# Optimization experiments

Hardware: AMD Instinct MI355X
Metric: run time of the kernel (lower is better)

## Reference

```python
import jax, jax.numpy as jnp
import numpy as np

IN_FEATURES = 2048
OUT_FEATURES = 4096
NUM_SHIFTS = 10  # perms


def setup_inputs() -> dict:
    key = jax.random.key(0)
    kx, kw = jax.random.split(key)
    x = jax.random.normal(kx, (4, 2048, IN_FEATURES), dtype=jnp.float32)
    # nn.Linear weight: (out_features, in_features), Kaiming-uniform-ish init
    bound = 1.0 / np.sqrt(IN_FEATURES)
    W = jax.random.uniform(kw, (OUT_FEATURES, IN_FEATURES), dtype=jnp.float32,
                           minval=-bound, maxval=bound)
    return {"x": x, "W": W}


def _combined_weight(W):
    # Wt: (in, out). Sum of all weight variants; sum_i(x @ W_i) == x @ sum_i(W_i).
    Wt = W.T
    Weff = Wt + jnp.flip(Wt, axis=0) + jnp.flip(Wt, axis=1)
    for i in range(NUM_SHIFTS // 2):
        Weff = Weff + jnp.roll(Wt, shift=i + 1, axis=1)
        Weff = Weff + jnp.roll(Wt, shift=i + 1, axis=0)
    return Weff  # (in, out)


def reference(x, W):
    # reg_out (x @ W.T) + flipped + rolled variants, collapsed into one GEMM
    Weff = _combined_weight(W)
    return jnp.einsum('bsi,io->bso', x, Weff)
```

## Files before the change

kernel.cpp:

```cpp
#include <hip/hip_runtime.h>
#include <hip/hip_bf16.h>
#include <stdint.h>

#define M_DIM 8192
#define K_DIM 2048
#define N_DIM 4096
#define BM 256
#define BN 256
#define BK 64
#define NT (K_DIM / BK)
#define NITER (NT / 2)

typedef __attribute__((ext_vector_type(8))) short bf16x8;
typedef __attribute__((ext_vector_type(4))) float f32x4;

__device__ __forceinline__ unsigned short f2bfu(float f) {
    __hip_bfloat16 h = __float2bfloat16(f);
    return __builtin_bit_cast(unsigned short, h);
}

__global__ __launch_bounds__(256) void prep_fused(const float* __restrict__ x,
                                                  const float* __restrict__ W,
                                                  unsigned short* __restrict__ xb,
                                                  unsigned short* __restrict__ wt) {
    const int bid = blockIdx.x;
    if (bid < N_DIM) {
        __shared__ float row[K_DIM];
        const int o = bid;
        const float* wo = W + (size_t)o * K_DIM;
#pragma unroll
        for (int t = 0; t < 2; ++t)
            ((float4*)row)[threadIdx.x + 256 * t] = ((const float4*)wo)[threadIdx.x + 256 * t];
        __syncthreads();

        const float* rF = W + (size_t)(N_DIM - 1 - o) * K_DIM;
        const float* r1 = W + (size_t)((o - 1) & (N_DIM - 1)) * K_DIM;
        const float* r2 = W + (size_t)((o - 2) & (N_DIM - 1)) * K_DIM;
        const float* r3 = W + (size_t)((o - 3) & (N_DIM - 1)) * K_DIM;
        const float* r4 = W + (size_t)((o - 4) & (N_DIM - 1)) * K_DIM;
        const float* r5 = W + (size_t)((o - 5) & (N_DIM - 1)) * K_DIM;
        unsigned short* w = wt + (size_t)o * K_DIM;

#pragma unroll
        for (int t = 0; t < 2; ++t) {
            const int i0 = (threadIdx.x + 256 * t) * 4;
            const float4 vF = *(const float4*)(rF + i0);
            const float4 v1 = *(const float4*)(r1 + i0);
            const float4 v2 = *(const float4*)(r2 + i0);
            const float4 v3 = *(const float4*)(r3 + i0);
            const float4 v4 = *(const float4*)(r4 + i0);
            const float4 v5 = *(const float4*)(r5 + i0);
            ushort4 ov;
#pragma unroll
            for (int j = 0; j < 4; ++j) {
                const int i = i0 + j;
                float s = row[i] + row[K_DIM - 1 - i]
                        + row[(i - 1) & (K_DIM - 1)] + row[(i - 2) & (K_DIM - 1)]
                        + row[(i - 3) & (K_DIM - 1)] + row[(i - 4) & (K_DIM - 1)]
                        + row[(i - 5) & (K_DIM - 1)];
                s += (&vF.x)[j] + (&v1.x)[j] + (&v2.x)[j]
                   + (&v3.x)[j] + (&v4.x)[j] + (&v5.x)[j];
                (&ov.x)[j] = f2bfu(s);
            }
            *(ushort4*)(w + i0) = ov;
        }
    } else {
        const int idx = (bid - N_DIM) * 256 + threadIdx.x;
        float4 v = ((const float4*)x)[idx];
        ushort4 o;
        o.x = f2bfu(v.x); o.y = f2bfu(v.y); o.z = f2bfu(v.z); o.w = f2bfu(v.w);
        ((ushort4*)xb)[idx] = o;
    }
}

__global__ __launch_bounds__(512, 2) void gemm8p(const unsigned short* __restrict__ Ab,
                                                 const unsigned short* __restrict__ Bt,
                                                 float* __restrict__ C) {
    __shared__ __align__(16) char smem[2 * 65536];

    const int tid  = threadIdx.x;
    const int wave = tid >> 6;
    const int lane = tid & 63;

    const int nwg = gridDim.x;
    const int cpx = nwg >> 3;
    const int wg  = (blockIdx.x & 7) * cpx + (blockIdx.x >> 3);
    const int nbn = N_DIM / BN;
    const int bm0 = (wg / nbn) * BM;
    const int bn0 = (wg % nbn) * BN;

    const int wr = wave >> 2;
    const int wc = wave & 3;

    const int srow = tid >> 3;
    const int lsw  = (lane & 7) ^ ((lane >> 3) & 7);
    const unsigned short* gA0 = Ab + (size_t)(bm0 + srow) * K_DIM + lsw * 8;
    const unsigned short* gB0 = Bt + (size_t)(bn0 + srow) * K_DIM + lsw * 8;

    const int r16  = lane & 15;
    const int x7   = lane & 7;
    const int ksl0 = (((lane >> 4)    ) ^ x7) * 16;
    const int ksl1 = (((lane >> 4) | 4) ^ x7) * 16;
    const int aRow = (wr * 128 + r16) * 128;
    const int bRow = (wc * 64  + r16) * 128 + 32768;

    f32x4  acc[8][4] = {};
    bf16x8 b[4][2];

#define STAGE_HALF(gbase, opoff, h, t, p) do {                                              \
    char* lds_ = smem + (p) * 65536 + (opoff) + (h) * 16384 + wave * 1024;                  \
    const unsigned short* g_ = (gbase) + (size_t)((h) * 128) * K_DIM + (t) * BK;            \
    __builtin_amdgcn_global_load_lds(                                                        \
        (const __attribute__((address_space(1))) unsigned int*)g_,                           \
        (__attribute__((address_space(3))) unsigned int*)lds_, 16, 0, 0);                    \
    __builtin_amdgcn_global_load_lds(                                                        \
        (const __attribute__((address_space(1))) unsigned int*)(g_ + (size_t)64 * K_DIM),    \
        (__attribute__((address_space(3))) unsigned int*)(lds_ + 8192), 16, 0, 0);           \
} while (0)

#define PHASE(P, Q, LOADB, STAGE_STMT, VM_STMT) do {                                        \
    const char* base_ = smem + (P) * 65536;                                                 \
    bf16x8 a_[2][2];                                                                        \
    if (LOADB) {                                                                            \
        _Pragma("unroll")                                                                   \
        for (int fn = 0; fn < 4; ++fn) {                                                    \
            b[fn][0] = *(const bf16x8*)(base_ + bRow + fn * 2048 + ksl0);                   \
            b[fn][1] = *(const bf16x8*)(base_ + bRow + fn * 2048 + ksl1);                   \
        }                                                                                   \
    }                                                                                       \
    a_[0][0] = *(const bf16x8*)(base_ + aRow + (Q) * 4096 + ksl0);                          \
    a_[0][1] = *(const bf16x8*)(base_ + aRow + (Q) * 4096 + ksl1);                          \
    a_[1][0] = *(const bf16x8*)(base_ + aRow + (Q) * 4096 + 2048 + ksl0);                   \
    a_[1][1] = *(const bf16x8*)(base_ + aRow + (Q) * 4096 + 2048 + ksl1);                   \
    STAGE_STMT;                                                                             \
    __builtin_amdgcn_s_barrier();                                                           \
    asm volatile("s_waitcnt lgkmcnt(0)" ::: "memory");                                      \
    __builtin_amdgcn_sched_barrier(0);                                                      \
    __builtin_amdgcn_s_setprio(1);                                                          \
    _Pragma("unroll")                                                                       \
    for (int fm = 0; fm < 2; ++fm)                                                          \
        _Pragma("unroll")                                                                   \
        for (int fn = 0; fn < 4; ++fn) {                                                    \
            acc[(Q)*2 + fm][fn] = __builtin_amdgcn_mfma_f32_16x16x32_bf16(                  \
                a_[fm][0], b[fn][0], acc[(Q)*2 + fm][fn], 0, 0, 0);                         \
            acc[(Q)*2 + fm][fn] = __builtin_amdgcn_mfma_f32_16x16x32_bf16(                  \
                a_[fm][1], b[fn][1], acc[(Q)*2 + fm][fn], 0, 0, 0);                         \
        }                                                                                   \
    __builtin_amdgcn_s_setprio(0);                                                          \
    VM_STMT;                                                                                \
    __builtin_amdgcn_s_barrier();                                                           \
} while (0)

    STAGE_HALF(gA0, 0,     0, 0, 0);
    STAGE_HALF(gA0, 0,     1, 0, 0);
    STAGE_HALF(gB0, 32768, 0, 0, 0);
    STAGE_HALF(gB0, 32768, 1, 0, 0);
    STAGE_HALF(gB0, 32768, 0, 1, 1);
    STAGE_HALF(gB0, 32768, 1, 1, 1);
    asm volatile("s_waitcnt vmcnt(4)" ::: "memory");
    __builtin_amdgcn_s_barrier();

    for (int u = 0; u < NITER; ++u) {
        const bool last = (u == NITER - 1);
        const int  t1 = 2 * u + 1, t2 = 2 * u + 2, t3 = 2 * u + 3;

        PHASE(0, 0, 1, { STAGE_HALF(gA0, 0, 0, t1, 1); }, {});
        PHASE(0, 1, 0, { STAGE_HALF(gA0, 0, 1, t1, 1); }, {});
        PHASE(0, 2, 0, { if (!last) STAGE_HALF(gB0, 32768, 0, t2, 0); }, {});
        PHASE(0, 3, 0, { if (!last) STAGE_HALF(gB0, 32768, 1, t2, 0); },
              { if (last) asm volatile("s_waitcnt vmcnt(0)" ::: "memory");
                else      asm volatile("s_waitcnt vmcnt(4)" ::: "memory"); });
        PHASE(1, 0, 1, { if (!last) STAGE_HALF(gA0, 0, 0, t2, 0); }, {});
        PHASE(1, 1, 0, { if (!last) STAGE_HALF(gA0, 0, 1, t2, 0); }, {});
        PHASE(1, 2, 0, { if (!last) STAGE_HALF(gB0, 32768, 0, t3, 1); }, {});
        PHASE(1, 3, 0, { if (!last) STAGE_HALF(gB0, 32768, 1, t3, 1); },
              { if (!last) asm volatile("s_waitcnt vmcnt(4)" ::: "memory"); });
    }
#undef PHASE
#undef STAGE_HALF

    const int crow = (lane >> 4) * 4;
    const int ccol = lane & 15;
    float* Cb = C + (size_t)(bm0 + wr * 128 + crow) * N_DIM + (bn0 + wc * 64 + ccol);
#pragma unroll
    for (int fm = 0; fm < 8; ++fm)
#pragma unroll
        for (int fn = 0; fn < 4; ++fn)
#pragma unroll
            for (int r = 0; r < 4; ++r)
                Cb[(size_t)(fm * 16 + r) * N_DIM + fn * 16] = acc[fm][fn][r];
}

extern "C" void kernel_launch(void* const* d_in, const int* in_sizes, int n_in,
                              void* d_out, int out_size, void* d_ws, size_t ws_size,
                              hipStream_t stream) {
    const float* x = (const float*)d_in[0];
    const float* W = (const float*)d_in[1];
    float* out = (float*)d_out;

    unsigned short* xb = (unsigned short*)d_ws;
    unsigned short* wt = (unsigned short*)((char*)d_ws + (size_t)M_DIM * K_DIM * 2);

    const int cvt_blocks = (M_DIM * K_DIM) / 4 / 256;
    prep_fused<<<N_DIM + cvt_blocks, 256, 0, stream>>>(x, W, xb, wt);

    dim3 grid((M_DIM / BM) * (N_DIM / BN));
    gemm8p<<<grid, 512, 0, stream>>>(xb, wt, out);
}
```

Measured before the change: 174.7 us.

## Process two weight rows per prep block and deepen GEMM prefetch schedule

The weight-combining prep kernel now handles two output rows per block. It reuses row0 as the shift-1 neighbour of row1 and shares the other shifted-row global loads, which cuts redundant reads of W. The GEMM main loop reorders its global-to-LDS staging so that B tiles are issued first and one A half-tile is prefetched a stage earlier, with the vmcnt waits raised from 4 to 6. This keeps more loads in flight, at the risk of LDS buffer hazards if the new ordering does not match the consumption order.

```diff
diff --git a/kernel.cpp b/kernel.cpp
--- a/kernel.cpp
+++ b/kernel.cpp
@@ -24,48 +24,64 @@
                                                   unsigned short* __restrict__ xb,
                                                   unsigned short* __restrict__ wt) {
     const int bid = blockIdx.x;
-    if (bid < N_DIM) {
-        __shared__ float row[K_DIM];
-        const int o = bid;
-        const float* wo = W + (size_t)o * K_DIM;
-#pragma unroll
-        for (int t = 0; t < 2; ++t)
-            ((float4*)row)[threadIdx.x + 256 * t] = ((const float4*)wo)[threadIdx.x + 256 * t];
+    if (bid < N_DIM / 2) {
+        __shared__ float row0[K_DIM];
+        __shared__ float row1[K_DIM];
+        const int o0 = bid * 2;
+        const float* w0 = W + (size_t)o0 * K_DIM;
+        const float* w1 = W + (size_t)(o0 + 1) * K_DIM;
+#pragma unroll
+        for (int t = 0; t < 2; ++t) {
+            ((float4*)row0)[threadIdx.x + 256 * t] = ((const float4*)w0)[threadIdx.x + 256 * t];
+            ((float4*)row1)[threadIdx.x + 256 * t] = ((const float4*)w1)[threadIdx.x + 256 * t];
+        }
         __syncthreads();
 
-        const float* rF = W + (size_t)(N_DIM - 1 - o) * K_DIM;
-        const float* r1 = W + (size_t)((o - 1) & (N_DIM - 1)) * K_DIM;
-        const float* r2 = W + (size_t)((o - 2) & (N_DIM - 1)) * K_DIM;
-        const float* r3 = W + (size_t)((o - 3) & (N_DIM - 1)) * K_DIM;
-        const float* r4 = W + (size_t)((o - 4) & (N_DIM - 1)) * K_DIM;
-        const float* r5 = W + (size_t)((o - 5) & (N_DIM - 1)) * K_DIM;
-        unsigned short* w = wt + (size_t)o * K_DIM;
+        const float* rF0 = W + (size_t)(N_DIM - 1 - o0) * K_DIM;
+        const float* rF1 = W + (size_t)(N_DIM - 2 - o0) * K_DIM;
+        const float* rm1 = W + (size_t)((o0 - 1) & (N_DIM - 1)) * K_DIM;
+        const float* rm2 = W + (size_t)((o0 - 2) & (N_DIM - 1)) * K_DIM;
+        const float* rm3 = W + (size_t)((o0 - 3) & (N_DIM - 1)) * K_DIM;
+        const float* rm4 = W + (size_t)((o0 - 4) & (N_DIM - 1)) * K_DIM;
+        const float* rm5 = W + (size_t)((o0 - 5) & (N_DIM - 1)) * K_DIM;
+        unsigned short* wo0 = wt + (size_t)o0 * K_DIM;
+        unsigned short* wo1 = wo0 + K_DIM;
 
 #pragma unroll
         for (int t = 0; t < 2; ++t) {
             const int i0 = (threadIdx.x + 256 * t) * 4;
-            const float4 vF = *(const float4*)(rF + i0);
-            const float4 v1 = *(const float4*)(r1 + i0);
-            const float4 v2 = *(const float4*)(r2 + i0);
-            const float4 v3 = *(const float4*)(r3 + i0);
-            const float4 v4 = *(const float4*)(r4 + i0);
-            const float4 v5 = *(const float4*)(r5 + i0);
-            ushort4 ov;
+            const float4 vF0 = *(const float4*)(rF0 + i0);
+            const float4 vF1 = *(const float4*)(rF1 + i0);
+            const float4 v1  = *(const float4*)(rm1 + i0);
+            const float4 v2  = *(const float4*)(rm2 + i0);
+            const float4 v3  = *(const float4*)(rm3 + i0);
+            const float4 v4  = *(const float4*)(rm4 + i0);
+            const float4 v5  = *(const float4*)(rm5 + i0);
+            ushort4 ov0, ov1;
 #pragma unroll
             for (int j = 0; j < 4; ++j) {
                 const int i = i0 + j;
-                float s = row[i] + row[K_DIM - 1 - i]
-                        + row[(i - 1) & (K_DIM - 1)] + row[(i - 2) & (K_DIM - 1)]
-                        + row[(i - 3) & (K_DIM - 1)] + row[(i - 4) & (K_DIM - 1)]
-                        + row[(i - 5) & (K_DIM - 1)];
-                s += (&vF.x)[j] + (&v1.x)[j] + (&v2.x)[j]
-                   + (&v3.x)[j] + (&v4.x)[j] + (&v5.x)[j];
-                (&ov.x)[j] = f2bfu(s);
+                float s0 = row0[i] + row0[K_DIM - 1 - i]
+                         + row0[(i - 1) & (K_DIM - 1)] + row0[(i - 2) & (K_DIM - 1)]
+                         + row0[(i - 3) & (K_DIM - 1)] + row0[(i - 4) & (K_DIM - 1)]
+                         + row0[(i - 5) & (K_DIM - 1)];
+                s0 += (&vF0.x)[j] + (&v1.x)[j] + (&v2.x)[j]
+                    + (&v3.x)[j] + (&v4.x)[j] + (&v5.x)[j];
+                (&ov0.x)[j] = f2bfu(s0);
+
+                float s1 = row1[i] + row1[K_DIM - 1 - i]
+                         + row1[(i - 1) & (K_DIM - 1)] + row1[(i - 2) & (K_DIM - 1)]
+                         + row1[(i - 3) & (K_DIM - 1)] + row1[(i - 4) & (K_DIM - 1)]
+                         + row1[(i - 5) & (K_DIM - 1)];
+                s1 += (&vF1.x)[j] + row0[i] + (&v1.x)[j] + (&v2.x)[j]
+                    + (&v3.x)[j] + (&v4.x)[j];
+                (&ov1.x)[j] = f2bfu(s1);
             }
-            *(ushort4*)(w + i0) = ov;
+            *(ushort4*)(wo0 + i0) = ov0;
+            *(ushort4*)(wo1 + i0) = ov1;
         }
     } else {
-        const int idx = (bid - N_DIM) * 256 + threadIdx.x;
+        const int idx = (bid - N_DIM / 2) * 256 + threadIdx.x;
         float4 v = ((const float4*)x)[idx];
         ushort4 o;
         o.x = f2bfu(v.x); o.y = f2bfu(v.y); o.z = f2bfu(v.z); o.w = f2bfu(v.w);
@@ -151,30 +167,31 @@
     __builtin_amdgcn_s_barrier();                                                           \
 } while (0)
 
+    STAGE_HALF(gB0, 32768, 0, 0, 0);
+    STAGE_HALF(gB0, 32768, 1, 0, 0);
     STAGE_HALF(gA0, 0,     0, 0, 0);
     STAGE_HALF(gA0, 0,     1, 0, 0);
-    STAGE_HALF(gB0, 32768, 0, 0, 0);
-    STAGE_HALF(gB0, 32768, 1, 0, 0);
     STAGE_HALF(gB0, 32768, 0, 1, 1);
     STAGE_HALF(gB0, 32768, 1, 1, 1);
-    asm volatile("s_waitcnt vmcnt(4)" ::: "memory");
+    STAGE_HALF(gA0, 0,     0, 1, 1);
+    asm volatile("s_waitcnt vmcnt(6)" ::: "memory");
     __builtin_amdgcn_s_barrier();
 
     for (int u = 0; u < NITER; ++u) {
         const bool last = (u == NITER - 1);
         const int  t1 = 2 * u + 1, t2 = 2 * u + 2, t3 = 2 * u + 3;
 
-        PHASE(0, 0, 1, { STAGE_HALF(gA0, 0, 0, t1, 1); }, {});
-        PHASE(0, 1, 0, { STAGE_HALF(gA0, 0, 1, t1, 1); }, {});
-        PHASE(0, 2, 0, { if (!last) STAGE_HALF(gB0, 32768, 0, t2, 0); }, {});
-        PHASE(0, 3, 0, { if (!last) STAGE_HALF(gB0, 32768, 1, t2, 0); },
+        PHASE(0, 0, 1, { STAGE_HALF(gA0, 0, 1, t1, 1); }, {});
+        PHASE(0, 1, 0, { if (!last) STAGE_HALF(gB0, 32768, 0, t2, 0); }, {});
+        PHASE(0, 2, 0, { if (!last) STAGE_HALF(gB0, 32768, 1, t2, 0); }, {});
+        PHASE(0, 3, 0, { if (!last) STAGE_HALF(gA0, 0, 0, t2, 0); },
               { if (last) asm volatile("s_waitcnt vmcnt(0)" ::: "memory");
-                else      asm volatile("s_waitcnt vmcnt(4)" ::: "memory"); });
-        PHASE(1, 0, 1, { if (!last) STAGE_HALF(gA0, 0, 0, t2, 0); }, {});
-        PHASE(1, 1, 0, { if (!last) STAGE_HALF(gA0, 0, 1, t2, 0); }, {});
-        PHASE(1, 2, 0, { if (!last) STAGE_HALF(gB0, 32768, 0, t3, 1); }, {});
-        PHASE(1, 3, 0, { if (!last) STAGE_HALF(gB0, 32768, 1, t3, 1); },
-              { if (!last) asm volatile("s_waitcnt vmcnt(4)" ::: "memory"); });
+                else      asm volatile("s_waitcnt vmcnt(6)" ::: "memory"); });
+        PHASE(1, 0, 1, { if (!last) STAGE_HALF(gA0, 0, 1, t2, 0); }, {});
+        PHASE(1, 1, 0, { if (!last) STAGE_HALF(gB0, 32768, 0, t3, 1); }, {});
+        PHASE(1, 2, 0, { if (!last) STAGE_HALF(gB0, 32768, 1, t3, 1); }, {});
+        PHASE(1, 3, 0, { if (!last) STAGE_HALF(gA0, 0, 0, t3, 1); },
+              { if (!last) asm volatile("s_waitcnt vmcnt(6)" ::: "memory"); });
     }
 #undef PHASE
 #undef STAGE_HALF
@@ -202,7 +219,7 @@
     unsigned short* wt = (unsigned short*)((char*)d_ws + (size_t)M_DIM * K_DIM * 2);
 
     const int cvt_blocks = (M_DIM * K_DIM) / 4 / 256;
-    prep_fused<<<N_DIM + cvt_blocks, 256, 0, stream>>>(x, W, xb, wt);
+    prep_fused<<<N_DIM / 2 + cvt_blocks, 256, 0, stream>>>(x, W, xb, wt);
 
     dim3 grid((M_DIM / BM) * (N_DIM / BN));
     gemm8p<<<grid, 512, 0, stream>>>(xb, wt, out);
```

New measurement: 163.6 us. 6.4% less time.
